# Kernel tuning notes

Hardware: AMD Instinct MI355X
Metric: run time of the kernel (lower is better)

Reference implementation:

```python
import jax, jax.numpy as jnp
import numpy as np

B, T, C, O = 32, 2048, 1152, 29  # batch, temporal len, in channels (sum(data_length)), classes


def setup_inputs() -> dict:
    key = jax.random.key(0)
    k1, k2, k3, k4 = jax.random.split(key, 4)
    x = jax.random.normal(k1, (B, T, C), dtype=jnp.float32)
    # per-sample valid length, >=1 to avoid div-by-zero
    length = jax.random.randint(k2, (B,), 1, T + 1, dtype=jnp.int64)
    # Conv1d(C, O, 1) weight [O, C, 1] -> stored as [O, C]; bias [O]
    W = jax.random.normal(k3, (O, C), dtype=jnp.float32) * (1.0 / np.sqrt(C))
    b = jax.random.normal(k4, (O,), dtype=jnp.float32) * 0.01
    return {"x": x, "length": length, "W": W, "b": b}


def reference(x, length, W, b):
    # x: [B, T, C]; scale/shift then 1x1 conv (pointwise linear) then sum over T.
    # Linearity lets us fuse: sum_t (W @ (x/64 - 2) + b) == einsum + T*b.
    y = x / 64.0 - 2.0                      # [B, T, C]
    z = jnp.einsum('btc,oc->bo', y, W)      # temporal-summed projection [B, O]
    z = z + jnp.asarray(x.shape[1], z.dtype) * b
    return z / length.astype(z.dtype)[:, None]
```

## Files before the change

### kernel.cpp

```cpp
#include <hip/hip_runtime.h>
#include <hip/hip_bf16.h>


#define PB 32
#define PT 2048
#define PC 1152
#define PO 29
#define TSPLIT 64
#define SLAB (PT / TSPLIT)
#define C4 (PC / 4)

typedef float f32x4 __attribute__((ext_vector_type(4)));

__global__ __launch_bounds__(256) void sum_t_kernel(const float* __restrict__ x,
                                                    float* __restrict__ part) {
    const int b   = blockIdx.x;
    const int p   = blockIdx.y;
    const int tid = threadIdx.x;

    const f32x4* x4 = (const f32x4*)(x + (size_t)b * PT * PC)
                    + (size_t)(p * SLAB) * C4;

    f32x4 a0 = (f32x4)(0.f);
    f32x4 a1 = (f32x4)(0.f);

#pragma unroll 8
    for (int t = 0; t < SLAB; ++t) {
        const f32x4* row = x4 + (size_t)t * C4;
        f32x4 v = __builtin_nontemporal_load(&row[tid]);
        a0 += v;
        if (tid < C4 - 256) {
            f32x4 v2 = __builtin_nontemporal_load(&row[256 + tid]);
            a1 += v2;
        }
    }

    f32x4* out4 = (f32x4*)(part + ((size_t)p * PB + b) * PC);
    out4[tid] = a0;
    if (tid < C4 - 256) out4[256 + tid] = a1;
}

__global__ __launch_bounds__(256) void reduce_proj_kernel(const float* __restrict__ part,
                                                          const float* __restrict__ W,
                                                          const float* __restrict__ bias,
                                                          const int* __restrict__ length,
                                                          float* __restrict__ out) {
    __shared__ float s[PC];
    const int b   = blockIdx.x;
    const int tid = threadIdx.x;

    const f32x4* part4 = (const f32x4*)part;
    for (int c4 = tid; c4 < C4; c4 += 256) {
        f32x4 acc = (f32x4)(0.f);
#pragma unroll 8
        for (int p = 0; p < TSPLIT; ++p) {
            acc += part4[((size_t)p * PB + b) * C4 + c4];
        }
        ((f32x4*)s)[c4] = acc;
    }
    __syncthreads();

    const int wave = tid >> 6;
    const int lane = tid & 63;
    const float invlen = 1.0f / (float)length[b];

    for (int o = wave; o < PO; o += 4) {
        const float* Wo = W + o * PC;
        float dot = 0.f, wsum = 0.f;
#pragma unroll
        for (int c = lane; c < PC; c += 64) {
            float w = Wo[c];
            dot  += w * s[c];
            wsum += w;
        }
#pragma unroll
        for (int off = 32; off > 0; off >>= 1) {
            dot  += __shfl_down(dot,  off);
            wsum += __shfl_down(wsum, off);
        }
        if (lane == 0) {
            float z = dot * (1.0f / 64.0f)
                    - 2.0f * (float)PT * wsum
                    + (float)PT * bias[o];
            out[b * PO + o] = z * invlen;
        }
    }
}

extern "C" void kernel_launch(void* const* d_in, const int* in_sizes, int n_in,
                              void* d_out, int out_size, void* d_ws, size_t ws_size,
                              hipStream_t stream) {
    const float* x      = (const float*)d_in[0];
    const int*   length = (const int*)d_in[1];
    const float* W      = (const float*)d_in[2];
    const float* bias   = (const float*)d_in[3];
    float*       out    = (float*)d_out;
    float*       part   = (float*)d_ws;

    dim3 g1(PB, TSPLIT);
    sum_t_kernel<<<g1, 256, 0, stream>>>(x, part);

    reduce_proj_kernel<<<PB, 256, 0, stream>>>(part, W, bias, length, out);
}
```

Baseline: 439.9 us.

## Fuse temporal sum and projection via last-block atomic counter

Merges the partial-sum kernel and the reduce/projection kernel into one launch. Each block bumps a per-batch atomic counter after writing its partial, and the last block for a batch does the cross-slab reduction and the projection. This removes a kernel launch and the gap between the two kernels, at the cost of a memset launch for the counters, atomics, and a serial tail on the last block per batch.

After: 516.2 us. 17.3% more time.

```diff
diff --git a/kernel.cpp b/kernel.cpp
--- a/kernel.cpp
+++ b/kernel.cpp
@@ -12,8 +12,13 @@
 
 typedef float f32x4 __attribute__((ext_vector_type(4)));
 
-__global__ __launch_bounds__(256) void sum_t_kernel(const float* __restrict__ x,
-                                                    float* __restrict__ part) {
+__global__ __launch_bounds__(256) void fused_kernel(const float* __restrict__ x,
+                                                    float* __restrict__ part,
+                                                    unsigned int* __restrict__ counters,
+                                                    const float* __restrict__ W,
+                                                    const float* __restrict__ bias,
+                                                    const int* __restrict__ length,
+                                                    float* __restrict__ out) {
     const int b   = blockIdx.x;
     const int p   = blockIdx.y;
     const int tid = threadIdx.x;
@@ -27,34 +32,36 @@
 #pragma unroll 8
     for (int t = 0; t < SLAB; ++t) {
         const f32x4* row = x4 + (size_t)t * C4;
-        f32x4 v = __builtin_nontemporal_load(&row[tid]);
-        a0 += v;
+        a0 += __builtin_nontemporal_load(&row[tid]);
         if (tid < C4 - 256) {
-            f32x4 v2 = __builtin_nontemporal_load(&row[256 + tid]);
-            a1 += v2;
+            a1 += __builtin_nontemporal_load(&row[256 + tid]);
         }
     }
 
     f32x4* out4 = (f32x4*)(part + ((size_t)p * PB + b) * PC);
     out4[tid] = a0;
     if (tid < C4 - 256) out4[256 + tid] = a1;
-}
 
-__global__ __launch_bounds__(256) void reduce_proj_kernel(const float* __restrict__ part,
-                                                          const float* __restrict__ W,
-                                                          const float* __restrict__ bias,
-                                                          const int* __restrict__ length,
-                                                          float* __restrict__ out) {
+    __shared__ int is_last;
+    __syncthreads();
+    if (tid == 0) {
+        unsigned int old = __hip_atomic_fetch_add(&counters[b], 1u,
+                                                  __ATOMIC_ACQ_REL,
+                                                  __HIP_MEMORY_SCOPE_AGENT);
+        is_last = (old == TSPLIT - 1);
+    }
+    __syncthreads();
+    if (!is_last) return;
+
+    __threadfence();
+
     __shared__ float s[PC];
-    const int b   = blockIdx.x;
-    const int tid = threadIdx.x;
-
     const f32x4* part4 = (const f32x4*)part;
     for (int c4 = tid; c4 < C4; c4 += 256) {
         f32x4 acc = (f32x4)(0.f);
 #pragma unroll 8
-        for (int p = 0; p < TSPLIT; ++p) {
-            acc += part4[((size_t)p * PB + b) * C4 + c4];
+        for (int pp = 0; pp < TSPLIT; ++pp) {
+            acc += part4[((size_t)pp * PB + b) * C4 + c4];
         }
         ((f32x4*)s)[c4] = acc;
     }
@@ -95,10 +102,12 @@
     const float* W      = (const float*)d_in[2];
     const float* bias   = (const float*)d_in[3];
     float*       out    = (float*)d_out;
-    float*       part   = (float*)d_ws;
 
-    dim3 g1(PB, TSPLIT);
-    sum_t_kernel<<<g1, 256, 0, stream>>>(x, part);
+    float*        part     = (float*)d_ws;
+    unsigned int* counters = (unsigned int*)((char*)d_ws + (size_t)TSPLIT * PB * PC * sizeof(float));
 
-    reduce_proj_kernel<<<PB, 256, 0, stream>>>(part, W, bias, length, out);
+    hipMemsetAsync(counters, 0, PB * sizeof(unsigned int), stream);
+
+    dim3 g(PB, TSPLIT);
+    fused_kernel<<<g, 256, 0, stream>>>(x, part, counters, W, bias, length, out);
 }
```
